# Optimization experiments

Hardware: AMD Instinct MI355X
Metric: run time of the kernel (lower is better)

## Reference

```python
import jax, jax.numpy as jnp
import numpy as np

B = 2048
WIDTH = 128      # channel width == 1D signal length after unsqueeze
MODES = 16       # retained Fourier modes
INPUT_DIM = 100
T_DIM = 28
U_DIM = 64
NFREQ = WIDTH // 2 + 1


def setup_inputs() -> dict:
    key = jax.random.key(0)
    ks = jax.random.split(key, 32)
    rn = lambda k, s: jax.random.normal(k, s, jnp.float32)
    un = lambda k, s: jax.random.uniform(k, s, jnp.float32)
    sc_in0 = 1.0 / (1 * WIDTH)        # SpectralConv scale for conv0 (in=1)
    sc_in = 1.0 / (WIDTH * WIDTH)     # for conv1..3
    inp = {
        "X1": rn(ks[0], (B, INPUT_DIM + T_DIM)),
        "fc0_w": rn(ks[1], (WIDTH, INPUT_DIM + T_DIM)) * 0.02,
        "fc0_b": jnp.zeros((WIDTH,), jnp.float32),
        # spectral weights: torch.rand(..., cfloat) -> uniform real & imag in [0,1), scaled
        "sc0_wr": un(ks[2], (1, WIDTH, MODES)) * sc_in0,
        "sc0_wi": un(ks[3], (1, WIDTH, MODES)) * sc_in0,
        "sc1_wr": un(ks[4], (WIDTH, WIDTH, MODES)) * sc_in,
        "sc1_wi": un(ks[5], (WIDTH, WIDTH, MODES)) * sc_in,
        "sc2_wr": un(ks[6], (WIDTH, WIDTH, MODES)) * sc_in,
        "sc2_wi": un(ks[7], (WIDTH, WIDTH, MODES)) * sc_in,
        "sc3_wr": un(ks[8], (WIDTH, WIDTH, MODES)) * sc_in,
        "sc3_wi": un(ks[9], (WIDTH, WIDTH, MODES)) * sc_in,
        # pointwise (kernel-size-1) Conv1d weights as [out, in] + bias
        "w0_w": rn(ks[10], (WIDTH, 1)) * 0.02,
        "w0_b": jnp.zeros((WIDTH,), jnp.float32),
        "w1_w": rn(ks[11], (WIDTH, WIDTH)) * 0.02,
        "w1_b": jnp.zeros((WIDTH,), jnp.float32),
        "w2_w": rn(ks[12], (WIDTH, WIDTH)) * 0.02,
        "w2_b": jnp.zeros((WIDTH,), jnp.float32),
        "w3_w": rn(ks[13], (WIDTH, WIDTH)) * 0.02,
        "w3_b": jnp.zeros((WIDTH,), jnp.float32),
        "fc1_w": rn(ks[14], (WIDTH, WIDTH * WIDTH)) * 0.01,
        "fc1_b": jnp.zeros((WIDTH,), jnp.float32),
        "fc2_w": rn(ks[15], (U_DIM, WIDTH)) * 0.02,
        "fc2_b": jnp.zeros((U_DIM,), jnp.float32),
    }
    return inp


def _spectral_conv(x, wr, wi):
    # x: [B, Cin, L]; wr/wi: [Cin, Cout, MODES]
    L = x.shape[-1]
    xf = jnp.fft.rfft(x)                                   # [B, Cin, L//2+1] complex
    w = wr + 1j * wi
    of = jnp.einsum('bim,iom->bom', xf[:, :, :MODES], w)   # [B, Cout, MODES]
    of = jnp.pad(of, ((0, 0), (0, 0), (0, L // 2 + 1 - MODES)))
    return jnp.fft.irfft(of, n=L)                          # [B, Cout, L] real


def _pointwise(x, w, b):
    # kernel-size-1 Conv1d: x [B, Cin, L], w [Cout, Cin], b [Cout]
    return jnp.einsum('bil,oi->bol', x, w) + b[None, :, None]


def _gelu(x):
    return jax.nn.gelu(x, approximate=False)  # torch F.gelu default (erf)


def reference(X1, fc0_w, fc0_b, sc0_wr, sc0_wi, sc1_wr, sc1_wi, sc2_wr, sc2_wi,
              sc3_wr, sc3_wi, w0_w, w0_b, w1_w, w1_b, w2_w, w2_b, w3_w, w3_b,
              fc1_w, fc1_b, fc2_w, fc2_b):
    # fc0: lift [B, input_dim+t_dim] -> [B, width]
    x = X1 @ fc0_w.T + fc0_b
    x = x[:, None, :]  # [B, 1, WIDTH]
    x = _gelu(_spectral_conv(x, sc0_wr, sc0_wi) + _pointwise(x, w0_w, w0_b))
    x = _gelu(_spectral_conv(x, sc1_wr, sc1_wi) + _pointwise(x, w1_w, w1_b))
    x = _gelu(_spectral_conv(x, sc2_wr, sc2_wi) + _pointwise(x, w2_w, w2_b))
    x = _spectral_conv(x, sc3_wr, sc3_wi) + _pointwise(x, w3_w, w3_b)
    x = x.reshape(x.shape[0], -1)              # [B, WIDTH*WIDTH]
    x = _gelu(x @ fc1_w.T + fc1_b)
    x = x @ fc2_w.T + fc2_b                    # [B, U_DIM]
    return jnp.squeeze(x)
```

## Files before the change

kernel.cpp:

```cpp
#include <hip/hip_runtime.h>
#include <math.h>

#define PI_D 3.14159265358979323846

#define OFF_TW   0u
#define OFF_X0   4096u
#define OFF_PWT  OFF_X0
#define OFF_TWT  (OFF_X0 + 49152u)
#define OFF_WT   (OFF_X0 + 262144u)
#define OFF_XFR  (OFF_WT + 1572864u)
#define OFF_XFI  (OFF_XFR + 4194304u)
#define OFF_OFR  (OFF_XFI + 4194304u)
#define OFF_OFI  (OFF_OFR + 4194304u)
#define OFF_A    (OFF_OFI + 4194304u)
#define OFF_HP   OFF_XFR

__device__ __forceinline__ float gelu_f(float x) {
    return 0.5f * x * (1.0f + erff(x * 0.7071067811865476f));
}

__device__ __forceinline__ int swzc(int c4) { return 4 * (c4 ^ ((c4 >> 3) & 3)); }

__global__ void k_setup(float* ws) {
    int id = blockIdx.x * 256 + threadIdx.x;
    if (id < 4096) {
        int l = id >> 5, c = id & 31, m = c & 15;
        double ang = (PI_D / 64.0) * (double)((m * l) & 127);
        double v = (c < 16) ? cos(ang) : -sin(ang);
        ws[OFF_TW + id] = (float)v;
    }
}

__global__ void k_transpose(const float* w1r, const float* w1i,
                            const float* w2r, const float* w2i,
                            const float* w3r, const float* w3i, float* ws) {
    int id = blockIdx.x * 256 + threadIdx.x;
    int lay = id >> 18;
    int rem = id & 262143;
    int m = rem >> 14, i = (rem >> 7) & 127, o = rem & 127;
    const float* sr = (lay == 0) ? w1r : (lay == 1) ? w2r : w3r;
    const float* si = (lay == 0) ? w1i : (lay == 1) ? w2i : w3i;
    int src = (i * 128 + o) * 16 + m;
    ws[OFF_WT + (unsigned)lay * 524288u + rem] = sr[src];
    ws[OFF_WT + (unsigned)lay * 524288u + 262144u + rem] = si[src];
}

__global__ void k_prep2(const float* w1w, const float* w2w, const float* w3w, float* ws) {
    int id = blockIdx.x * 256 + threadIdx.x;
    if (id < 49152) {
        int lay = id >> 14, rem = id & 16383;
        int i = rem >> 7, o = rem & 127;
        const float* w = (lay == 0) ? w1w : (lay == 1) ? w2w : w3w;
        ws[OFF_PWT + id] = w[o * 128 + i];
    } else if (id < 53248) {
        int id2 = id - 49152;
        int c = id2 >> 7, l = id2 & 127;
        ws[OFF_TWT + c * 128 + l] = ws[OFF_TW + l * 32 + c];
    }
}

__global__ __launch_bounds__(256) void k_fc0(const float* X1, const float* w, const float* bias, float* ws) {
    __shared__ float xs[16][128];
    __shared__ float wsm[128][129];
    int t = threadIdx.x;
    int b0 = blockIdx.x * 16;
#pragma unroll
    for (int q = 0; q < 8; ++q) {
        int idx = q * 256 + t;
        xs[idx >> 7][idx & 127] = X1[b0 * 128 + idx];
    }
#pragma unroll
    for (int q = 0; q < 64; ++q) {
        int idx = q * 256 + t;
        wsm[idx >> 7][idx & 127] = w[idx];
    }
    __syncthreads();
    int c = t & 127, bh = t >> 7;
    float* x0 = ws + OFF_X0;
    for (int j = 0; j < 8; ++j) {
        int b = bh * 8 + j;
        float acc = bias[c];
#pragma unroll 8
        for (int k = 0; k < 128; ++k) acc += xs[b][k] * wsm[c][k];
        x0[(b0 + b) * 128 + c] = acc;
    }
}

__global__ __launch_bounds__(256) void k_layer0(const float* w0r, const float* w0i,
                                                const float* w0w, const float* w0b, float* ws) {
    __shared__ float x0s[128];
    __shared__ float tws[128][33];
    __shared__ float xrs[16], xis[16];
    __shared__ __align__(16) float ors[2048];
    __shared__ __align__(16) float ois[2048];
    int t = threadIdx.x, b = blockIdx.x;
    const float* tw = ws + OFF_TW;
    const float* x0 = ws + OFF_X0;
    if (t < 128) x0s[t] = x0[b * 128 + t];
#pragma unroll
    for (int q = 0; q < 16; ++q) {
        int idx = q * 256 + t;
        tws[idx >> 5][idx & 31] = tw[idx];
    }
    __syncthreads();
    if (t < 32) {
        float acc = 0.f;
        for (int l = 0; l < 128; ++l) acc += x0s[l] * tws[l][t];
        if (t < 16) xrs[t] = acc; else xis[t - 16] = acc;
    }
    __syncthreads();
#pragma unroll
    for (int q = 0; q < 8; ++q) {
        int idx = q * 256 + t;
        int m = idx & 15;
        float wr = w0r[idx], wi = w0i[idx];
        float sc = (m == 0) ? (1.f / 128.f) : (2.f / 128.f);
        float xr = xrs[m], xi = xis[m];
        ors[idx] = (xr * wr - xi * wi) * sc;
        ois[idx] = (xr * wi + xi * wr) * sc;
    }
    __syncthreads();
    int l = t & 127, og = t >> 7;
    float tvc[16], tvs[16];
#pragma unroll
    for (int m = 0; m < 16; ++m) { tvc[m] = tws[l][m]; tvs[m] = tws[l][16 + m]; }
    float xl = x0s[l];
    float* A = ws + OFF_A + b * 16384;
    const float4* or4 = (const float4*)ors;
    const float4* oi4 = (const float4*)ois;
    for (int oj = 0; oj < 64; ++oj) {
        int o = og * 64 + oj;
        float acc = xl * w0w[o] + w0b[o];
#pragma unroll
        for (int q = 0; q < 4; ++q) {
            float4 r4 = or4[o * 4 + q];
            float4 i4 = oi4[o * 4 + q];
            acc += r4.x * tvc[4 * q + 0] + i4.x * tvs[4 * q + 0];
            acc += r4.y * tvc[4 * q + 1] + i4.y * tvs[4 * q + 1];
            acc += r4.z * tvc[4 * q + 2] + i4.z * tvs[4 * q + 2];
            acc += r4.w * tvc[4 * q + 3] + i4.w * tvs[4 * q + 3];
        }
        A[o * 128 + l] = gelu_f(acc);
    }
}

__global__ __launch_bounds__(128) void k_dft(float* ws) {
    __shared__ float as_[16][260];
    __shared__ float tws_[16][32];
    int t = threadIdx.x;
    int row0 = blockIdx.x * 256;
    const float* A = ws + OFF_A;
    const float* tw = ws + OFF_TW;
    int tr = t >> 2, tc = t & 3;
    float acc[8][8];
#pragma unroll
    for (int j = 0; j < 8; ++j)
#pragma unroll
        for (int cc = 0; cc < 8; ++cc) acc[j][cc] = 0.f;
    int col0 = swzc(2 * tr), col1 = swzc(2 * tr + 1);
    for (int kc = 0; kc < 8; ++kc) {
        int k0 = kc * 16;
        if (kc) __syncthreads();
#pragma unroll
        for (int q = 0; q < 8; ++q) {
            int idx = q * 128 + t;
            int r = idx >> 2, kq = idx & 3;
            float4 v = *(const float4*)&A[(row0 + r) * 128 + k0 + 4 * kq];
            int sc = swzc(r >> 2) + (r & 3);
            as_[4 * kq + 0][sc] = v.x; as_[4 * kq + 1][sc] = v.y;
            as_[4 * kq + 2][sc] = v.z; as_[4 * kq + 3][sc] = v.w;
        }
#pragma unroll
        for (int q = 0; q < 4; ++q) {
            int idx = q * 128 + t;
            tws_[idx >> 5][idx & 31] = tw[(k0 + (idx >> 5)) * 32 + (idx & 31)];
        }
        __syncthreads();
#pragma unroll 8
        for (int kk = 0; kk < 16; ++kk) {
            float4 a0 = *(const float4*)&as_[kk][col0];
            float4 a1 = *(const float4*)&as_[kk][col1];
            float4 t0 = *(const float4*)&tws_[kk][tc * 8];
            float4 t1 = *(const float4*)&tws_[kk][tc * 8 + 4];
            float av[8] = {a0.x,a0.y,a0.z,a0.w,a1.x,a1.y,a1.z,a1.w};
            float tv[8] = {t0.x,t0.y,t0.z,t0.w,t1.x,t1.y,t1.z,t1.w};
#pragma unroll
            for (int j = 0; j < 8; ++j)
#pragma unroll
                for (int cc = 0; cc < 8; ++cc) acc[j][cc] += av[j] * tv[cc];
        }
    }
    float* xfr = ws + OFF_XFR;
    float* xfi = ws + OFF_XFI;
#pragma unroll
    for (int cc = 0; cc < 8; ++cc) {
        int c = tc * 8 + cc;
        float* dst = (c < 16) ? (xfr + c * 262144) : (xfi + (c - 16) * 262144);
        float4 v0 = make_float4(acc[0][cc], acc[1][cc], acc[2][cc], acc[3][cc]);
        float4 v1 = make_float4(acc[4][cc], acc[5][cc], acc[6][cc], acc[7][cc]);
        *(float4*)&dst[row0 + tr * 8] = v0;
        *(float4*)&dst[row0 + tr * 8 + 4] = v1;
    }
}

__global__ __launch_bounds__(256) void k_modemix(int lay, float* ws) {
    __shared__ float xrs[32][68], xis[32][68];
    __shared__ float wrs[32][132], wis[32][132];
    int t = threadIdx.x;
    int b0 = blockIdx.x * 64;
    int m = blockIdx.y;
    const float* xfr = ws + OFF_XFR + m * 262144;
    const float* xfi = ws + OFF_XFI + m * 262144;
    const float* wtr = ws + OFF_WT + (unsigned)lay * 524288u + m * 16384;
    const float* wti = wtr + 262144;
    int tb = t >> 4, tc = t & 15;
    int wc0 = swzc(2 * tc), wc1 = swzc(2 * tc + 1);
    float accr[4][8], acci[4][8];
#pragma unroll
    for (int jb = 0; jb < 4; ++jb)
#pragma unroll
        for (int jc = 0; jc < 8; ++jc) { accr[jb][jc] = 0.f; acci[jb][jc] = 0.f; }
    for (int kc = 0; kc < 4; ++kc) {
        int k0 = kc * 32;
        if (kc) __syncthreads();
#pragma unroll
        for (int q = 0; q < 2; ++q) {
            int idx = q * 256 + t;
            int r = idx >> 3, kq = idx & 7;
            float4 vr = *(const float4*)&xfr[(b0 + r) * 128 + k0 + 4 * kq];
            float4 vi = *(const float4*)&xfi[(b0 + r) * 128 + k0 + 4 * kq];
            xrs[4*kq+0][r] = vr.x; xrs[4*kq+1][r] = vr.y; xrs[4*kq+2][r] = vr.z; xrs[4*kq+3][r] = vr.w;
            xis[4*kq+0][r] = vi.x; xis[4*kq+1][r] = vi.y; xis[4*kq+2][r] = vi.z; xis[4*kq+3][r] = vi.w;
        }
#pragma unroll
        for (int q = 0; q < 4; ++q) {
            int idx = q * 256 + t;
            int kk = idx >> 5, oq = idx & 31;
            *(float4*)&wrs[kk][swzc(oq)] = *(const float4*)&wtr[(k0 + kk) * 128 + 4 * oq];
            *(float4*)&wis[kk][swzc(oq)] = *(const float4*)&wti[(k0 + kk) * 128 + 4 * oq];
        }
        __syncthreads();
#pragma unroll 4
        for (int kk = 0; kk < 32; ++kk) {
            float4 xr4 = *(const float4*)&xrs[kk][tb * 4];
            float4 xi4 = *(const float4*)&xis[kk][tb * 4];
            float4 wr0 = *(const float4*)&wrs[kk][wc0];
            float4 wr1 = *(const float4*)&wrs[kk][wc1];
            float4 wi0 = *(const float4*)&wis[kk][wc0];
            float4 wi1 = *(const float4*)&wis[kk][wc1];
            float xrv[4] = {xr4.x, xr4.y, xr4.z, xr4.w};
            float xiv[4] = {xi4.x, xi4.y, xi4.z, xi4.w};
            float wrv[8] = {wr0.x,wr0.y,wr0.z,wr0.w,wr1.x,wr1.y,wr1.z,wr1.w};
            float wiv[8] = {wi0.x,wi0.y,wi0.z,wi0.w,wi1.x,wi1.y,wi1.z,wi1.w};
#pragma unroll
            for (int jb = 0; jb < 4; ++jb)
#pragma unroll
                for (int jc = 0; jc < 8; ++jc) {
                    accr[jb][jc] += xrv[jb] * wrv[jc] - xiv[jb] * wiv[jc];
                    acci[jb][jc] += xrv[jb] * wiv[jc] + xiv[jb] * wrv[jc];
                }
        }
    }
    float* ofr = ws + OFF_OFR + m * 262144;
    float* ofi = ws + OFF_OFI + m * 262144;
#pragma unroll
    for (int jb = 0; jb < 4; ++jb) {
        int b = b0 + tb * 4 + jb;
        float4 r0 = make_float4(accr[jb][0], accr[jb][1], accr[jb][2], accr[jb][3]);
        float4 r1 = make_float4(accr[jb][4], accr[jb][5], accr[jb][6], accr[jb][7]);
        float4 i0 = make_float4(acci[jb][0], acci[jb][1], acci[jb][2], acci[jb][3]);
        float4 i1 = make_float4(acci[jb][4], acci[jb][5], acci[jb][6], acci[jb][7]);
        *(float4*)&ofr[b * 128 + tc * 8]     = r0;
        *(float4*)&ofr[b * 128 + tc * 8 + 4] = r1;
        *(float4*)&ofi[b * 128 + tc * 8]     = i0;
        *(float4*)&ofi[b * 128 + tc * 8 + 4] = i1;
    }
}

template <int GELU>
__global__ __launch_bounds__(256) void k_layerB(const float* pwt, const float* pw_b, float* ws) {
    __shared__ float smem[8448];
    int t = threadIdx.x, b = blockIdx.x;
    float* A = ws + OFF_A + (unsigned)b * 16384u;
    const float* ofr = ws + OFF_OFR;
    const float* ofi = ws + OFF_OFI;
    const float* twt = ws + OFF_TWT;
    int ty = t >> 4, tx = t & 15;
    int col0 = swzc(2 * tx), col1 = swzc(2 * tx + 1);
    float* ofr_s = smem;
    float* ofi_s = smem + 2048;
    float* twTs  = smem + 4096;
#pragma unroll
    for (int q = 0; q < 2; ++q) {
        int idx = q * 256 + t;
        int mm = idx >> 5, oq = idx & 31;
        float sc = (mm == 0) ? (1.f / 128.f) : (2.f / 128.f);
        float4 vr = *(const float4*)&ofr[mm * 262144 + b * 128 + 4 * oq];
        float4 vi = *(const float4*)&ofi[mm * 262144 + b * 128 + 4 * oq];
        vr.x *= sc; vr.y *= sc; vr.z *= sc; vr.w *= sc;
        vi.x *= sc; vi.y *= sc; vi.z *= sc; vi.w *= sc;
        *(float4*)&ofr_s[mm * 128 + 4 * oq] = vr;
        *(float4*)&ofi_s[mm * 128 + 4 * oq] = vi;
    }
#pragma unroll
    for (int q = 0; q < 4; ++q) {
        int idx = q * 256 + t;
        int row = idx >> 5, c4 = idx & 31;
        *(float4*)&twTs[row * 132 + swzc(c4)] = *(const float4*)&twt[row * 128 + 4 * c4];
    }
    __syncthreads();
    float acc[8][8];
#pragma unroll
    for (int jo = 0; jo < 8; ++jo)
#pragma unroll
        for (int jl = 0; jl < 8; ++jl) acc[jo][jl] = 0.f;
#pragma unroll 2
    for (int m = 0; m < 16; ++m) {
        float4 or0 = *(const float4*)&ofr_s[m * 128 + ty * 8];
        float4 or1 = *(const float4*)&ofr_s[m * 128 + ty * 8 + 4];
        float4 oi0 = *(const float4*)&ofi_s[m * 128 + ty * 8];
        float4 oi1 = *(const float4*)&ofi_s[m * 128 + ty * 8 + 4];
        float4 c0 = *(const float4*)&twTs[m * 132 + col0];
        float4 c1 = *(const float4*)&twTs[m * 132 + col1];
        float4 s0 = *(const float4*)&twTs[(16 + m) * 132 + col0];
        float4 s1 = *(const float4*)&twTs[(16 + m) * 132 + col1];
        float orv[8] = {or0.x,or0.y,or0.z,or0.w,or1.x,or1.y,or1.z,or1.w};
        float oiv[8] = {oi0.x,oi0.y,oi0.z,oi0.w,oi1.x,oi1.y,oi1.z,oi1.w};
        float cv[8]  = {c0.x,c0.y,c0.z,c0.w,c1.x,c1.y,c1.z,c1.w};
        float sv[8]  = {s0.x,s0.y,s0.z,s0.w,s1.x,s1.y,s1.z,s1.w};
#pragma unroll
        for (int jo = 0; jo < 8; ++jo)
#pragma unroll
            for (int jl = 0; jl < 8; ++jl) acc[jo][jl] += orv[jo] * cv[jl] + oiv[jo] * sv[jl];
    }
    __syncthreads();
    float* as_ = smem;
    float* wsx = smem + 4224;
    for (int ch = 0; ch < 4; ++ch) {
        int i0 = ch * 32;
        if (ch) __syncthreads();
#pragma unroll
        for (int q = 0; q < 4; ++q) {
            int idx = q * 256 + t;
            int ic = idx >> 5, lq = idx & 31;
            *(float4*)&as_[ic * 132 + swzc(lq)] = *(const float4*)&A[(i0 + ic) * 128 + 4 * lq];
        }
#pragma unroll
        for (int q = 0; q < 4; ++q) {
            int idx = q * 256 + t;
            int ic = idx >> 5, oq = idx & 31;
            *(float4*)&wsx[ic * 132 + 4 * oq] = *(const float4*)&pwt[(i0 + ic) * 128 + 4 * oq];
        }
        __syncthreads();
#pragma unroll 4
        for (int ic = 0; ic < 32; ++ic) {
            float4 a0 = *(const float4*)&as_[ic * 132 + col0];
            float4 a1 = *(const float4*)&as_[ic * 132 + col1];
            float4 w0 = *(const float4*)&wsx[ic * 132 + ty * 8];
            float4 w1 = *(const float4*)&wsx[ic * 132 + ty * 8 + 4];
            float av[8] = {a0.x,a0.y,a0.z,a0.w,a1.x,a1.y,a1.z,a1.w};
            float wv[8] = {w0.x,w0.y,w0.z,w0.w,w1.x,w1.y,w1.z,w1.w};
#pragma unroll
            for (int jo = 0; jo < 8; ++jo)
#pragma unroll
                for (int jl = 0; jl < 8; ++jl) acc[jo][jl] += wv[jo] * av[jl];
        }
    }
#pragma unroll
    for (int jo = 0; jo < 8; ++jo) {
        int o = ty * 8 + jo;
        float bv = pw_b[o];
        float v[8];
#pragma unroll
        for (int jl = 0; jl < 8; ++jl) {
            float x = acc[jo][jl] + bv;
            v[jl] = GELU ? gelu_f(x) : x;
        }
        *(float4*)&A[o * 128 + tx * 8]     = make_float4(v[0], v[1], v[2], v[3]);
        *(float4*)&A[o * 128 + tx * 8 + 4] = make_float4(v[4], v[5], v[6], v[7]);
    }
}

__global__ __launch_bounds__(256) void k_fc12(const float* fc1w, float* ws) {
    __shared__ float as_[32][132];
    __shared__ float ws_[32][132];
    int t = threadIdx.x;
    int b0 = blockIdx.x * 128;
    int kz = blockIdx.y;
    const float* A = ws + OFF_A;
    int tm = t >> 4, tn = t & 15;
    int wc0 = swzc(2 * tn), wc1 = swzc(2 * tn + 1);
    float acc[8][8];
#pragma unroll
    for (int jb = 0; jb < 8; ++jb)
#pragma unroll
        for (int jc = 0; jc < 8; ++jc) acc[jb][jc] = 0.f;
    for (int ks = 0; ks < 8; ++ks) {
        int k0 = kz * 256 + ks * 32;
        if (ks) __syncthreads();
#pragma unroll
        for (int q = 0; q < 4; ++q) {
            int idx = q * 256 + t;
            int r = idx >> 3, kq = idx & 7;
            float4 v = *(const float4*)&A[(b0 + r) * 16384 + k0 + 4 * kq];
            as_[4*kq+0][r] = v.x; as_[4*kq+1][r] = v.y; as_[4*kq+2][r] = v.z; as_[4*kq+3][r] = v.w;
        }
#pragma unroll
        for (int q = 0; q < 4; ++q) {
            int idx = q * 256 + t;
            int c = idx >> 3, kq = idx & 7;
            float4 v = *(const float4*)&fc1w[c * 16384 + k0 + 4 * kq];
            int sc = swzc(c >> 2) + (c & 3);
            ws_[4*kq+0][sc] = v.x; ws_[4*kq+1][sc] = v.y; ws_[4*kq+2][sc] = v.z; ws_[4*kq+3][sc] = v.w;
        }
        __syncthreads();
#pragma unroll 4
        for (int kk = 0; kk < 32; ++kk) {
            float4 a0 = *(const float4*)&as_[kk][tm * 8];
            float4 a1 = *(const float4*)&as_[kk][tm * 8 + 4];
            float4 w0 = *(const float4*)&ws_[kk][wc0];
            float4 w1 = *(const float4*)&ws_[kk][wc1];
            float av[8] = {a0.x,a0.y,a0.z,a0.w,a1.x,a1.y,a1.z,a1.w};
            float wv[8] = {w0.x,w0.y,w0.z,w0.w,w1.x,w1.y,w1.z,w1.w};
#pragma unroll
            for (int jb = 0; jb < 8; ++jb)
#pragma unroll
                for (int jc = 0; jc < 8; ++jc) acc[jb][jc] += av[jb] * wv[jc];
        }
    }
    float* hp = ws + OFF_HP + kz * 262144;
#pragma unroll
    for (int jb = 0; jb < 8; ++jb) {
        int b = b0 + tm * 8 + jb;
        *(float4*)&hp[b * 128 + tn * 8]     = make_float4(acc[jb][0], acc[jb][1], acc[jb][2], acc[jb][3]);
        *(float4*)&hp[b * 128 + tn * 8 + 4] = make_float4(acc[jb][4], acc[jb][5], acc[jb][6], acc[jb][7]);
    }
}

__global__ __launch_bounds__(256) void k_fc2(const float* fc1b, const float* fc2w, const float* fc2b,
                                             float* ws, float* out) {
    __shared__ float hs[8][128];
    __shared__ float w2s[64][129];
    int t = threadIdx.x;
    int b0 = blockIdx.x * 8;
    const float* hp = ws + OFF_HP;
#pragma unroll
    for (int q = 0; q < 4; ++q) {
        int idx = q * 256 + t;
        int bb = idx >> 7, c = idx & 127;
        float s = fc1b[c];
#pragma unroll 8
        for (int kz = 0; kz < 64; ++kz) s += hp[kz * 262144 + (b0 + bb) * 128 + c];
        hs[bb][c] = gelu_f(s);
    }
#pragma unroll
    for (int q = 0; q < 32; ++q) {
        int idx = q * 256 + t;
        w2s[idx >> 7][idx & 127] = fc2w[idx];
    }
    __syncthreads();
#pragma unroll
    for (int q = 0; q < 2; ++q) {
        int idx = q * 256 + t;
        int bb = idx >> 6, u = idx & 63;
        float acc = fc2b[u];
#pragma unroll 8
        for (int c = 0; c < 128; ++c) acc += hs[bb][c] * w2s[u][c];
        out[(b0 + bb) * 64 + u] = acc;
    }
}

extern "C" void kernel_launch(void* const* d_in, const int* in_sizes, int n_in,
                              void* d_out, int out_size, void* d_ws, size_t ws_size,
                              hipStream_t stream) {
    const float* X1   = (const float*)d_in[0];
    const float* fc0w = (const float*)d_in[1];
    const float* fc0b = (const float*)d_in[2];
    const float* s0r  = (const float*)d_in[3];
    const float* s0i  = (const float*)d_in[4];
    const float* s1r  = (const float*)d_in[5];
    const float* s1i  = (const float*)d_in[6];
    const float* s2r  = (const float*)d_in[7];
    const float* s2i  = (const float*)d_in[8];
    const float* s3r  = (const float*)d_in[9];
    const float* s3i  = (const float*)d_in[10];
    const float* w0w  = (const float*)d_in[11];
    const float* w0b  = (const float*)d_in[12];
    const float* w1w  = (const float*)d_in[13];
    const float* w1b  = (const float*)d_in[14];
    const float* w2w  = (const float*)d_in[15];
    const float* w2b  = (const float*)d_in[16];
    const float* w3w  = (const float*)d_in[17];
    const float* w3b  = (const float*)d_in[18];
    const float* fc1w = (const float*)d_in[19];
    const float* fc1b = (const float*)d_in[20];
    const float* fc2w = (const float*)d_in[21];
    const float* fc2b = (const float*)d_in[22];
    float* ws  = (float*)d_ws;
    float* out = (float*)d_out;

    k_setup<<<dim3(16), dim3(256), 0, stream>>>(ws);
    k_transpose<<<dim3(3072), dim3(256), 0, stream>>>(s1r, s1i, s2r, s2i, s3r, s3i, ws);
    k_fc0<<<dim3(128), dim3(256), 0, stream>>>(X1, fc0w, fc0b, ws);
    k_layer0<<<dim3(2048), dim3(256), 0, stream>>>(s0r, s0i, w0w, w0b, ws);
    k_prep2<<<dim3(208), dim3(256), 0, stream>>>(w1w, w2w, w3w, ws);

    const float* pwb[3] = {w1b, w2b, w3b};
    for (int lay = 0; lay < 3; ++lay) {
        k_dft<<<dim3(1024), dim3(128), 0, stream>>>(ws);
        k_modemix<<<dim3(32, 16), dim3(256), 0, stream>>>(lay, ws);
        const float* pwt = ws + OFF_PWT + (unsigned)lay * 16384u;
        if (lay < 2)
            k_layerB<1><<<dim3(2048), dim3(256), 0, stream>>>(pwt, pwb[lay], ws);
        else
            k_layerB<0><<<dim3(2048), dim3(256), 0, stream>>>(pwt, pwb[lay], ws);
    }

    k_fc12<<<dim3(16, 64), dim3(256), 0, stream>>>(fc1w, ws);
    k_fc2<<<dim3(256), dim3(256), 0, stream>>>(fc1b, fc2w, fc2b, ws, out);
}
```

Baseline: 1.100 ms.

## Double-buffer shared-memory tiles with register prefetch in modemix, layerB and fc12 GEMMs

Converts the three main GEMM-style kernels (mode mixing, pointwise conv, fc1) from single-buffered 32-wide K chunks into double-buffered 16-wide chunks. The next chunk is loaded from global into registers while the current chunk is computed from shared memory, then written into the alternate buffer, leaving one barrier per step. This is meant to hide global load latency behind the FMA loops. In exchange it adds registers for the prefetched values, doubles the number of K steps, and changes the fc12 A-tile shared layout to a swizzled one.

Result: slower. 1.136 ms (+3.3%).

```diff
diff --git a/kernel.cpp b/kernel.cpp
--- a/kernel.cpp
+++ b/kernel.cpp
@@ -204,8 +204,7 @@
 }
 
 __global__ __launch_bounds__(256) void k_modemix(int lay, float* ws) {
-    __shared__ float xrs[32][68], xis[32][68];
-    __shared__ float wrs[32][132], wis[32][132];
+    __shared__ float smem[12800];
     int t = threadIdx.x;
     int b0 = blockIdx.x * 64;
     int m = blockIdx.y;
@@ -215,39 +214,57 @@
     const float* wti = wtr + 262144;
     int tb = t >> 4, tc = t & 15;
     int wc0 = swzc(2 * tc), wc1 = swzc(2 * tc + 1);
+    int xr_ = t >> 2, xkq = t & 3;
+    int wk0 = t >> 5, wo0 = t & 31;
+    int wk1 = 8 + wk0;
+    int wsl = swzc(wo0);
     float accr[4][8], acci[4][8];
 #pragma unroll
     for (int jb = 0; jb < 4; ++jb)
 #pragma unroll
         for (int jc = 0; jc < 8; ++jc) { accr[jb][jc] = 0.f; acci[jb][jc] = 0.f; }
-    for (int kc = 0; kc < 4; ++kc) {
-        int k0 = kc * 32;
-        if (kc) __syncthreads();
-#pragma unroll
-        for (int q = 0; q < 2; ++q) {
-            int idx = q * 256 + t;
-            int r = idx >> 3, kq = idx & 7;
-            float4 vr = *(const float4*)&xfr[(b0 + r) * 128 + k0 + 4 * kq];
-            float4 vi = *(const float4*)&xfi[(b0 + r) * 128 + k0 + 4 * kq];
-            xrs[4*kq+0][r] = vr.x; xrs[4*kq+1][r] = vr.y; xrs[4*kq+2][r] = vr.z; xrs[4*kq+3][r] = vr.w;
-            xis[4*kq+0][r] = vi.x; xis[4*kq+1][r] = vi.y; xis[4*kq+2][r] = vi.z; xis[4*kq+3][r] = vi.w;
-        }
-#pragma unroll
-        for (int q = 0; q < 4; ++q) {
-            int idx = q * 256 + t;
-            int kk = idx >> 5, oq = idx & 31;
-            *(float4*)&wrs[kk][swzc(oq)] = *(const float4*)&wtr[(k0 + kk) * 128 + 4 * oq];
-            *(float4*)&wis[kk][swzc(oq)] = *(const float4*)&wti[(k0 + kk) * 128 + 4 * oq];
-        }
-        __syncthreads();
+    float4 vxr = *(const float4*)&xfr[(b0 + xr_) * 128 + 4 * xkq];
+    float4 vxi = *(const float4*)&xfi[(b0 + xr_) * 128 + 4 * xkq];
+    float4 vwr0 = *(const float4*)&wtr[wk0 * 128 + 4 * wo0];
+    float4 vwr1 = *(const float4*)&wtr[wk1 * 128 + 4 * wo0];
+    float4 vwi0 = *(const float4*)&wti[wk0 * 128 + 4 * wo0];
+    float4 vwi1 = *(const float4*)&wti[wk1 * 128 + 4 * wo0];
+    {
+        float* xr = smem; float* xi = smem + 2176;
+        xr[(4*xkq+0)*68 + xr_] = vxr.x; xr[(4*xkq+1)*68 + xr_] = vxr.y;
+        xr[(4*xkq+2)*68 + xr_] = vxr.z; xr[(4*xkq+3)*68 + xr_] = vxr.w;
+        xi[(4*xkq+0)*68 + xr_] = vxi.x; xi[(4*xkq+1)*68 + xr_] = vxi.y;
+        xi[(4*xkq+2)*68 + xr_] = vxi.z; xi[(4*xkq+3)*68 + xr_] = vxi.w;
+        *(float4*)&smem[4352 + wk0 * 132 + wsl] = vwr0;
+        *(float4*)&smem[4352 + wk1 * 132 + wsl] = vwr1;
+        *(float4*)&smem[8576 + wk0 * 132 + wsl] = vwi0;
+        *(float4*)&smem[8576 + wk1 * 132 + wsl] = vwi1;
+    }
+    __syncthreads();
+    for (int ch = 0; ch < 8; ++ch) {
+        int xo = (ch & 1) * 1088;
+        int wo = (ch & 1) * 2112;
+        const float* cxr = smem + xo;
+        const float* cxi = smem + 2176 + xo;
+        const float* cwr = smem + 4352 + wo;
+        const float* cwi = smem + 8576 + wo;
+        if (ch < 7) {
+            int k0 = (ch + 1) * 16;
+            vxr = *(const float4*)&xfr[(b0 + xr_) * 128 + k0 + 4 * xkq];
+            vxi = *(const float4*)&xfi[(b0 + xr_) * 128 + k0 + 4 * xkq];
+            vwr0 = *(const float4*)&wtr[(k0 + wk0) * 128 + 4 * wo0];
+            vwr1 = *(const float4*)&wtr[(k0 + wk1) * 128 + 4 * wo0];
+            vwi0 = *(const float4*)&wti[(k0 + wk0) * 128 + 4 * wo0];
+            vwi1 = *(const float4*)&wti[(k0 + wk1) * 128 + 4 * wo0];
+        }
 #pragma unroll 4
-        for (int kk = 0; kk < 32; ++kk) {
-            float4 xr4 = *(const float4*)&xrs[kk][tb * 4];
-            float4 xi4 = *(const float4*)&xis[kk][tb * 4];
-            float4 wr0 = *(const float4*)&wrs[kk][wc0];
-            float4 wr1 = *(const float4*)&wrs[kk][wc1];
-            float4 wi0 = *(const float4*)&wis[kk][wc0];
-            float4 wi1 = *(const float4*)&wis[kk][wc1];
+        for (int kk = 0; kk < 16; ++kk) {
+            float4 xr4 = *(const float4*)&cxr[kk * 68 + tb * 4];
+            float4 xi4 = *(const float4*)&cxi[kk * 68 + tb * 4];
+            float4 wr0 = *(const float4*)&cwr[kk * 132 + wc0];
+            float4 wr1 = *(const float4*)&cwr[kk * 132 + wc1];
+            float4 wi0 = *(const float4*)&cwi[kk * 132 + wc0];
+            float4 wi1 = *(const float4*)&cwi[kk * 132 + wc1];
             float xrv[4] = {xr4.x, xr4.y, xr4.z, xr4.w};
             float xiv[4] = {xi4.x, xi4.y, xi4.z, xi4.w};
             float wrv[8] = {wr0.x,wr0.y,wr0.z,wr0.w,wr1.x,wr1.y,wr1.z,wr1.w};
@@ -259,6 +276,21 @@
                     accr[jb][jc] += xrv[jb] * wrv[jc] - xiv[jb] * wiv[jc];
                     acci[jb][jc] += xrv[jb] * wiv[jc] + xiv[jb] * wrv[jc];
                 }
+        }
+        if (ch < 7) {
+            int nxo = ((ch & 1) ^ 1) * 1088;
+            int nwo = ((ch & 1) ^ 1) * 2112;
+            float* nxr = smem + nxo;
+            float* nxi = smem + 2176 + nxo;
+            nxr[(4*xkq+0)*68 + xr_] = vxr.x; nxr[(4*xkq+1)*68 + xr_] = vxr.y;
+            nxr[(4*xkq+2)*68 + xr_] = vxr.z; nxr[(4*xkq+3)*68 + xr_] = vxr.w;
+            nxi[(4*xkq+0)*68 + xr_] = vxi.x; nxi[(4*xkq+1)*68 + xr_] = vxi.y;
+            nxi[(4*xkq+2)*68 + xr_] = vxi.z; nxi[(4*xkq+3)*68 + xr_] = vxi.w;
+            *(float4*)&smem[4352 + nwo + wk0 * 132 + wsl] = vwr0;
+            *(float4*)&smem[4352 + nwo + wk1 * 132 + wsl] = vwr1;
+            *(float4*)&smem[8576 + nwo + wk0 * 132 + wsl] = vwi0;
+            *(float4*)&smem[8576 + nwo + wk1 * 132 + wsl] = vwi1;
+            __syncthreads();
         }
     }
     float* ofr = ws + OFF_OFR + m * 262144;
@@ -287,6 +319,12 @@
     const float* twt = ws + OFF_TWT;
     int ty = t >> 4, tx = t & 15;
     int col0 = swzc(2 * tx), col1 = swzc(2 * tx + 1);
+    int r0 = t >> 5, r1 = 8 + (t >> 5), lq = t & 31;
+    int wslot = swzc(lq);
+    float4 pa0 = *(const float4*)&A[r0 * 128 + 4 * lq];
+    float4 pa1 = *(const float4*)&A[r1 * 128 + 4 * lq];
+    float4 pw0 = *(const float4*)&pwt[r0 * 128 + 4 * lq];
+    float4 pw1 = *(const float4*)&pwt[r1 * 128 + 4 * lq];
     float* ofr_s = smem;
     float* ofi_s = smem + 2048;
     float* twTs  = smem + 4096;
@@ -334,36 +372,42 @@
             for (int jl = 0; jl < 8; ++jl) acc[jo][jl] += orv[jo] * cv[jl] + oiv[jo] * sv[jl];
     }
     __syncthreads();
-    float* as_ = smem;
-    float* wsx = smem + 4224;
-    for (int ch = 0; ch < 4; ++ch) {
-        int i0 = ch * 32;
-        if (ch) __syncthreads();
-#pragma unroll
-        for (int q = 0; q < 4; ++q) {
-            int idx = q * 256 + t;
-            int ic = idx >> 5, lq = idx & 31;
-            *(float4*)&as_[ic * 132 + swzc(lq)] = *(const float4*)&A[(i0 + ic) * 128 + 4 * lq];
-        }
-#pragma unroll
-        for (int q = 0; q < 4; ++q) {
-            int idx = q * 256 + t;
-            int ic = idx >> 5, oq = idx & 31;
-            *(float4*)&wsx[ic * 132 + 4 * oq] = *(const float4*)&pwt[(i0 + ic) * 128 + 4 * oq];
-        }
-        __syncthreads();
+    *(float4*)&smem[r0 * 132 + wslot] = pa0;
+    *(float4*)&smem[r1 * 132 + wslot] = pa1;
+    *(float4*)&smem[4224 + r0 * 132 + 4 * lq] = pw0;
+    *(float4*)&smem[4224 + r1 * 132 + 4 * lq] = pw1;
+    __syncthreads();
+    for (int ch = 0; ch < 8; ++ch) {
+        int bo = (ch & 1) * 2112;
+        const float* cas = smem + bo;
+        const float* cwx = smem + 4224 + bo;
+        if (ch < 7) {
+            int i0 = (ch + 1) * 16;
+            pa0 = *(const float4*)&A[(i0 + r0) * 128 + 4 * lq];
+            pa1 = *(const float4*)&A[(i0 + r1) * 128 + 4 * lq];
+            pw0 = *(const float4*)&pwt[(i0 + r0) * 128 + 4 * lq];
+            pw1 = *(const float4*)&pwt[(i0 + r1) * 128 + 4 * lq];
+        }
 #pragma unroll 4
-        for (int ic = 0; ic < 32; ++ic) {
-            float4 a0 = *(const float4*)&as_[ic * 132 + col0];
-            float4 a1 = *(const float4*)&as_[ic * 132 + col1];
-            float4 w0 = *(const float4*)&wsx[ic * 132 + ty * 8];
-            float4 w1 = *(const float4*)&wsx[ic * 132 + ty * 8 + 4];
+        for (int ic = 0; ic < 16; ++ic) {
+            float4 a0 = *(const float4*)&cas[ic * 132 + col0];
+            float4 a1 = *(const float4*)&cas[ic * 132 + col1];
+            float4 w0 = *(const float4*)&cwx[ic * 132 + ty * 8];
+            float4 w1 = *(const float4*)&cwx[ic * 132 + ty * 8 + 4];
             float av[8] = {a0.x,a0.y,a0.z,a0.w,a1.x,a1.y,a1.z,a1.w};
             float wv[8] = {w0.x,w0.y,w0.z,w0.w,w1.x,w1.y,w1.z,w1.w};
 #pragma unroll
             for (int jo = 0; jo < 8; ++jo)
 #pragma unroll
                 for (int jl = 0; jl < 8; ++jl) acc[jo][jl] += wv[jo] * av[jl];
+        }
+        if (ch < 7) {
+            int nbo = ((ch & 1) ^ 1) * 2112;
+            *(float4*)&smem[nbo + r0 * 132 + wslot] = pa0;
+            *(float4*)&smem[nbo + r1 * 132 + wslot] = pa1;
+            *(float4*)&smem[4224 + nbo + r0 * 132 + 4 * lq] = pw0;
+            *(float4*)&smem[4224 + nbo + r1 * 132 + 4 * lq] = pw1;
+            __syncthreads();
         }
     }
 #pragma unroll
@@ -382,50 +426,73 @@
 }
 
 __global__ __launch_bounds__(256) void k_fc12(const float* fc1w, float* ws) {
-    __shared__ float as_[32][132];
-    __shared__ float ws_[32][132];
+    __shared__ float smem[8448];
     int t = threadIdx.x;
     int b0 = blockIdx.x * 128;
     int kz = blockIdx.y;
     const float* A = ws + OFF_A;
     int tm = t >> 4, tn = t & 15;
+    int ac0 = swzc(2 * tm), ac1 = swzc(2 * tm + 1);
     int wc0 = swzc(2 * tn), wc1 = swzc(2 * tn + 1);
+    int rr0 = t >> 2, rr1 = 64 + (t >> 2), kq = t & 3;
+    int sl0 = swzc(rr0 >> 2) + (rr0 & 3);
+    int sl1 = swzc(rr1 >> 2) + (rr1 & 3);
     float acc[8][8];
 #pragma unroll
     for (int jb = 0; jb < 8; ++jb)
 #pragma unroll
         for (int jc = 0; jc < 8; ++jc) acc[jb][jc] = 0.f;
-    for (int ks = 0; ks < 8; ++ks) {
-        int k0 = kz * 256 + ks * 32;
-        if (ks) __syncthreads();
-#pragma unroll
-        for (int q = 0; q < 4; ++q) {
-            int idx = q * 256 + t;
-            int r = idx >> 3, kq = idx & 7;
-            float4 v = *(const float4*)&A[(b0 + r) * 16384 + k0 + 4 * kq];
-            as_[4*kq+0][r] = v.x; as_[4*kq+1][r] = v.y; as_[4*kq+2][r] = v.z; as_[4*kq+3][r] = v.w;
-        }
-#pragma unroll
-        for (int q = 0; q < 4; ++q) {
-            int idx = q * 256 + t;
-            int c = idx >> 3, kq = idx & 7;
-            float4 v = *(const float4*)&fc1w[c * 16384 + k0 + 4 * kq];
-            int sc = swzc(c >> 2) + (c & 3);
-            ws_[4*kq+0][sc] = v.x; ws_[4*kq+1][sc] = v.y; ws_[4*kq+2][sc] = v.z; ws_[4*kq+3][sc] = v.w;
-        }
-        __syncthreads();
+    int kbase = kz * 256;
+    float4 va0 = *(const float4*)&A[(b0 + rr0) * 16384 + kbase + 4 * kq];
+    float4 va1 = *(const float4*)&A[(b0 + rr1) * 16384 + kbase + 4 * kq];
+    float4 vw0 = *(const float4*)&fc1w[rr0 * 16384 + kbase + 4 * kq];
+    float4 vw1 = *(const float4*)&fc1w[rr1 * 16384 + kbase + 4 * kq];
+    {
+        smem[(4*kq+0)*132 + sl0] = va0.x; smem[(4*kq+1)*132 + sl0] = va0.y;
+        smem[(4*kq+2)*132 + sl0] = va0.z; smem[(4*kq+3)*132 + sl0] = va0.w;
+        smem[(4*kq+0)*132 + sl1] = va1.x; smem[(4*kq+1)*132 + sl1] = va1.y;
+        smem[(4*kq+2)*132 + sl1] = va1.z; smem[(4*kq+3)*132 + sl1] = va1.w;
+        smem[4224 + (4*kq+0)*132 + sl0] = vw0.x; smem[4224 + (4*kq+1)*132 + sl0] = vw0.y;
+        smem[4224 + (4*kq+2)*132 + sl0] = vw0.z; smem[4224 + (4*kq+3)*132 + sl0] = vw0.w;
+        smem[4224 + (4*kq+0)*132 + sl1] = vw1.x; smem[4224 + (4*kq+1)*132 + sl1] = vw1.y;
+        smem[4224 + (4*kq+2)*132 + sl1] = vw1.z; smem[4224 + (4*kq+3)*132 + sl1] = vw1.w;
+    }
+    __syncthreads();
+    for (int ks = 0; ks < 16; ++ks) {
+        int bo = (ks & 1) * 2112;
+        const float* ca = smem + bo;
+        const float* cw = smem + 4224 + bo;
+        if (ks < 15) {
+            int k0 = kbase + (ks + 1) * 16;
+            va0 = *(const float4*)&A[(b0 + rr0) * 16384 + k0 + 4 * kq];
+            va1 = *(const float4*)&A[(b0 + rr1) * 16384 + k0 + 4 * kq];
+            vw0 = *(const float4*)&fc1w[rr0 * 16384 + k0 + 4 * kq];
+            vw1 = *(const float4*)&fc1w[rr1 * 16384 + k0 + 4 * kq];
+        }
 #pragma unroll 4
-        for (int kk = 0; kk < 32; ++kk) {
-            float4 a0 = *(const float4*)&as_[kk][tm * 8];
-            float4 a1 = *(const float4*)&as_[kk][tm * 8 + 4];
-            float4 w0 = *(const float4*)&ws_[kk][wc0];
-            float4 w1 = *(const float4*)&ws_[kk][wc1];
+        for (int kk = 0; kk < 16; ++kk) {
+            float4 a0 = *(const float4*)&ca[kk * 132 + ac0];
+            float4 a1 = *(const float4*)&ca[kk * 132 + ac1];
+            float4 w0 = *(const float4*)&cw[kk * 132 + wc0];
+            float4 w1 = *(const float4*)&cw[kk * 132 + wc1];
             float av[8] = {a0.x,a0.y,a0.z,a0.w,a1.x,a1.y,a1.z,a1.w};
             float wv[8] = {w0.x,w0.y,w0.z,w0.w,w1.x,w1.y,w1.z,w1.w};
 #pragma unroll
             for (int jb = 0; jb < 8; ++jb)
 #pragma unroll
                 for (int jc = 0; jc < 8; ++jc) acc[jb][jc] += av[jb] * wv[jc];
+        }
+        if (ks < 15) {
+            int nbo = ((ks & 1) ^ 1) * 2112;
+            smem[nbo + (4*kq+0)*132 + sl0] = va0.x; smem[nbo + (4*kq+1)*132 + sl0] = va0.y;
+            smem[nbo + (4*kq+2)*132 + sl0] = va0.z; smem[nbo + (4*kq+3)*132 + sl0] = va0.w;
+            smem[nbo + (4*kq+0)*132 + sl1] = va1.x; smem[nbo + (4*kq+1)*132 + sl1] = va1.y;
+            smem[nbo + (4*kq+2)*132 + sl1] = va1.z; smem[nbo + (4*kq+3)*132 + sl1] = va1.w;
+            smem[4224 + nbo + (4*kq+0)*132 + sl0] = vw0.x; smem[4224 + nbo + (4*kq+1)*132 + sl0] = vw0.y;
+            smem[4224 + nbo + (4*kq+2)*132 + sl0] = vw0.z; smem[4224 + nbo + (4*kq+3)*132 + sl0] = vw0.w;
+            smem[4224 + nbo + (4*kq+0)*132 + sl1] = vw1.x; smem[4224 + nbo + (4*kq+1)*132 + sl1] = vw1.y;
+            smem[4224 + nbo + (4*kq+2)*132 + sl1] = vw1.z; smem[4224 + nbo + (4*kq+3)*132 + sl1] = vw1.w;
+            __syncthreads();
         }
     }
     float* hp = ws + OFF_HP + kz * 262144;
```
